# Kernel optimization log

Measured on AMD Instinct MI355X. Metric: run time of the kernel, lower is better.

## Reference

```python
import jax, jax.numpy as jnp
import numpy as np
from jax import lax

KERNEL_SIZE = 3  # matches init_kwargs


def setup_inputs() -> dict:
    key = jax.random.key(0)
    heatmap = jax.random.normal(key, (8, 16, 512, 512), dtype=jnp.float32)
    return {"heatmap": heatmap, "max_peaks": 262144}


def reference(heatmap, max_peaks):
    """Peak detection: local maxima of 3x3 neighborhood that are > 0.

    Returns:
      peaks:  (B, max_peaks, 3) float32, rows [x, y, confidence] packed in
              (channel, row-major) order (identical ordering to the torch
              per-channel torch.where + cat), zero-padded after counts[b].
      counts: (B,) int32, number of valid peak rows per batch item.
    """
    k = KERNEL_SIZE
    pad = (k - 1) // 2
    # max_pool2d(stride=1, padding=pad) pads with -inf implicitly
    max_pooled = lax.reduce_window(
        heatmap, -jnp.inf, lax.max,
        window_dimensions=(1, 1, k, k),
        window_strides=(1, 1, 1, 1),
        padding=[(0, 0), (0, 0), (pad, pad), (pad, pad)],
    )
    peak_mask = (heatmap == max_pooled) & (heatmap > 0)

    B, C, H, W = heatmap.shape
    n = C * H * W
    flat_mask = peak_mask.reshape(B, n)
    flat_val = heatmap.reshape(B, n)

    # Stream compaction: stable argsort moves valid flat indices (in order)
    # to the front; invalid entries get sentinel key n.
    idx = jnp.arange(n, dtype=jnp.int32)
    keys = jnp.where(flat_mask, idx, jnp.int32(n))
    order = jnp.argsort(keys, axis=1)[:, :max_peaks]  # (B, max_peaks)

    valid = jnp.take_along_axis(flat_mask, order, axis=1)
    conf = jnp.take_along_axis(flat_val, order, axis=1)
    x = (order % W).astype(heatmap.dtype)
    y = ((order // W) % H).astype(heatmap.dtype)

    peaks = jnp.where(valid[..., None], jnp.stack([x, y, conf], axis=-1), 0.0)
    counts = flat_mask.sum(axis=1).astype(jnp.int32)
    return peaks, counts
```

## Files before the change

kernel.cpp:

```cpp
#include <hip/hip_runtime.h>


namespace {
constexpr int kB = 8;
constexpr int kC = 16;
constexpr int kH = 512;
constexpr int kW = 512;
constexpr int kNPB = kC * kH * kW;
constexpr int kMaxPeaks = 262144;
constexpr int kRows = 8;
constexpr int kStripsPerBatch = kC * (kH / kRows);
constexpr int kNStrips = kB * kStripsPerBatch;
constexpr int kWPB = 4;
constexpr int kTPB = 64 * kWPB;
constexpr long long kPeaksElems = (long long)kB * kMaxPeaks * 3;
constexpr float kNeg = -3.402823466e38f;
}

__device__ __forceinline__ float fmax3(float a, float b, float c) {
  return fmaxf(fmaxf(a, b), c);
}

__global__ void __launch_bounds__(kTPB)
peak_count_kernel(const float* __restrict__ hm,
                  unsigned long long* __restrict__ bmw,
                  int* __restrict__ cnts) {
  const int t = threadIdx.x, lane = t & 63, wv = t >> 6;
  const int s = blockIdx.x * kWPB + wv;
  const int b = s >> 10;
  const int si = s & 1023;
  const int c = si >> 6;
  const int y0 = (si & 63) * kRows;
  const float* rp = hm + (long long)b * kNPB + c * (kH * kW) + y0 * kW + lane * 8;

  float a[10][8];
#pragma unroll
  for (int i = 1; i <= 8; ++i) {
    const float4 q0 = *reinterpret_cast<const float4*>(rp + (i - 1) * kW);
    const float4 q1 = *reinterpret_cast<const float4*>(rp + (i - 1) * kW + 4);
    a[i][0] = q0.x; a[i][1] = q0.y; a[i][2] = q0.z; a[i][3] = q0.w;
    a[i][4] = q1.x; a[i][5] = q1.y; a[i][6] = q1.z; a[i][7] = q1.w;
  }
  if (y0 > 0) {
    const float4 q0 = *reinterpret_cast<const float4*>(rp - kW);
    const float4 q1 = *reinterpret_cast<const float4*>(rp - kW + 4);
    a[0][0] = q0.x; a[0][1] = q0.y; a[0][2] = q0.z; a[0][3] = q0.w;
    a[0][4] = q1.x; a[0][5] = q1.y; a[0][6] = q1.z; a[0][7] = q1.w;
  } else {
#pragma unroll
    for (int j = 0; j < 8; ++j) a[0][j] = kNeg;
  }
  if (y0 + kRows < kH) {
    const float4 q0 = *reinterpret_cast<const float4*>(rp + 8 * kW);
    const float4 q1 = *reinterpret_cast<const float4*>(rp + 8 * kW + 4);
    a[9][0] = q0.x; a[9][1] = q0.y; a[9][2] = q0.z; a[9][3] = q0.w;
    a[9][4] = q1.x; a[9][5] = q1.y; a[9][6] = q1.z; a[9][7] = q1.w;
  } else {
#pragma unroll
    for (int j = 0; j < 8; ++j) a[9][j] = kNeg;
  }

  unsigned long long myword = 0;
  int scnt = 0;
#pragma unroll
  for (int r = 0; r < kRows; ++r) {
    float cm[8];
#pragma unroll
    for (int j = 0; j < 8; ++j) cm[j] = fmax3(a[r][j], a[r + 1][j], a[r + 2][j]);
    float hl = __shfl_up(cm[7], 1, 64);
    float hr = __shfl_down(cm[0], 1, 64);
    if (lane == 0) hl = kNeg;
    if (lane == 63) hr = kNeg;
    float m[8];
    m[0] = fmax3(hl, cm[0], cm[1]);
#pragma unroll
    for (int j = 1; j < 7; ++j) m[j] = fmax3(cm[j - 1], cm[j], cm[j + 1]);
    m[7] = fmax3(cm[6], cm[7], hr);
#pragma unroll
    for (int j = 0; j < 8; ++j) {
      const float v = a[r + 1][j];
      const unsigned long long wj = __ballot((v == m[j]) && (v > 0.0f));
      scnt += (int)__popcll(wj);
      if (lane == r * 8 + j) myword = wj;
    }
  }
  bmw[(long long)s * 64 + lane] = myword;
  if (lane == 0) cnts[s] = scnt;
}

__global__ void __launch_bounds__(kTPB)
peak_write_kernel(const float* __restrict__ hm,
                  const unsigned long long* __restrict__ bmw,
                  const int* __restrict__ cnts,
                  float* __restrict__ out) {
  __shared__ int s_pre[kWPB], s_tot[kWPB], s_c[kWPB];
  __shared__ unsigned long long s_w[kWPB][64];
  const int t = threadIdx.x, lane = t & 63, wv = t >> 6;
  const int g = blockIdx.x;
  const int b = g >> 8;
  const int g0 = (g & 255) * kWPB;
  const int* cb = cnts + b * kStripsPerBatch;

  const int4 c4 = *reinterpret_cast<const int4*>(cb + t * 4);
  const int idx0 = t * 4;
  int tot = c4.x + c4.y + c4.z + c4.w;
  int pre = (idx0 < g0) ? tot : 0;
  if (idx0 == g0) { s_c[0] = c4.x; s_c[1] = c4.y; s_c[2] = c4.z; s_c[3] = c4.w; }
#pragma unroll
  for (int d = 32; d >= 1; d >>= 1) {
    pre += __shfl_down(pre, d, 64);
    tot += __shfl_down(tot, d, 64);
  }
  if (lane == 0) { s_pre[wv] = pre; s_tot[wv] = tot; }
  __syncthreads();
  const int base = s_pre[0] + s_pre[1] + s_pre[2] + s_pre[3];
  if (g0 == 0 && t == 0)
    out[kPeaksElems + b] =
        (float)(s_tot[0] + s_tot[1] + s_tot[2] + s_tot[3]);

  int off0 = base;
  for (int k = 0; k < wv; ++k) off0 += s_c[k];
  if (off0 >= kMaxPeaks) return;

  const int s = b * kStripsPerBatch + g0 + wv;
  const int si = g0 + wv, c = si >> 6, y0 = (si & 63) * kRows;
  const float* rp = hm + (long long)b * kNPB + c * (kH * kW) + y0 * kW + lane * 8;

  float4 cv[kRows][2];
#pragma unroll
  for (int r = 0; r < kRows; ++r) {
    cv[r][0] = *reinterpret_cast<const float4*>(rp + r * kW);
    cv[r][1] = *reinterpret_cast<const float4*>(rp + r * kW + 4);
  }

  s_w[wv][lane] = bmw[(long long)s * 64 + lane];

  const unsigned long long pm = (lane == 0) ? 0ull : (~0ull >> (64 - lane));
  int rbase = off0;
  float* pb = out + (long long)b * kMaxPeaks * 3;
#pragma unroll
  for (int r = 0; r < kRows; ++r) {
    unsigned long long w[8];
#pragma unroll
    for (int j = 0; j < 8; ++j) w[j] = s_w[wv][r * 8 + j];
    int lexcl = 0, rowcnt = 0;
#pragma unroll
    for (int j = 0; j < 8; ++j) {
      lexcl += (int)__popcll(w[j] & pm);
      rowcnt += (int)__popcll(w[j]);
    }
    int rank = rbase + lexcl;
    const float vv[8] = {cv[r][0].x, cv[r][0].y, cv[r][0].z, cv[r][0].w,
                         cv[r][1].x, cv[r][1].y, cv[r][1].z, cv[r][1].w};
    const float fy = (float)(y0 + r);
#pragma unroll
    for (int j = 0; j < 8; ++j) {
      const int f = (int)((w[j] >> lane) & 1);
      if (f && rank < kMaxPeaks) {
        float* o = pb + (long long)rank * 3;
        o[0] = (float)(lane * 8 + j);
        o[1] = fy;
        o[2] = vv[j];
      }
      rank += f;
    }
    rbase += rowcnt;
    if (rbase >= kMaxPeaks) break;
  }
}

extern "C" void kernel_launch(void* const* d_in, const int* in_sizes, int n_in,
                              void* d_out, int out_size, void* d_ws, size_t ws_size,
                              hipStream_t stream) {
  const float* hm = (const float*)d_in[0];
  float* out = (float*)d_out;

  unsigned long long* bmw = (unsigned long long*)d_ws;
  int* cnts = (int*)(bmw + (long long)kNStrips * 64);

  peak_count_kernel<<<kNStrips / kWPB, kTPB, 0, stream>>>(hm, bmw, cnts);
  peak_write_kernel<<<kNStrips / kWPB, kTPB, 0, stream>>>(hm, bmw, cnts, out);
}
```

Baseline: 220.3 us.

## Fuse count and write kernels with a grid-wide atomic barrier

Merges the peak-count and peak-write kernels into one persistent-style kernel. Each block handles 16 strips and keeps the peak bitmasks in shared memory instead of global memory. It publishes per-strip counts globally, then waits at a spin barrier on an atomic counter before doing the prefix sum and scatter. This removes the second launch and the bitmask round trip through global memory. The risks are deadlock if all 512 blocks are not co-resident, spin overhead at the barrier, and an extra memset launch.

Measured after the change: 310.2 us. +40.8%, slower.

```diff
diff --git a/kernel.cpp b/kernel.cpp
--- a/kernel.cpp
+++ b/kernel.cpp
@@ -11,8 +11,11 @@
 constexpr int kRows = 8;
 constexpr int kStripsPerBatch = kC * (kH / kRows);
 constexpr int kNStrips = kB * kStripsPerBatch;
-constexpr int kWPB = 4;
-constexpr int kTPB = 64 * kWPB;
+constexpr int kSPB = 16;
+constexpr int kNBlocks = kNStrips / kSPB;
+constexpr int kBlocksPerBatch = kStripsPerBatch / kSPB;
+constexpr int kTPB = 256;
+constexpr int kCntStride = 32;
 constexpr long long kPeaksElems = (long long)kB * kMaxPeaks * 3;
 constexpr float kNeg = -3.402823466e38f;
 }
@@ -21,151 +24,171 @@
   return fmaxf(fmaxf(a, b), c);
 }
 
-__global__ void __launch_bounds__(kTPB)
-peak_count_kernel(const float* __restrict__ hm,
-                  unsigned long long* __restrict__ bmw,
-                  int* __restrict__ cnts) {
+__global__ void __launch_bounds__(kTPB, 2)
+peak_fused(const float* __restrict__ hm, unsigned* __restrict__ bar,
+           int* __restrict__ cntg, float* __restrict__ out) {
+  __shared__ unsigned long long s_w[kSPB][64];
+  __shared__ int s_cnt[kSPB];
+  __shared__ int s_red[kTPB / 64], s_red2[kTPB / 64];
+
   const int t = threadIdx.x, lane = t & 63, wv = t >> 6;
-  const int s = blockIdx.x * kWPB + wv;
-  const int b = s >> 10;
-  const int si = s & 1023;
-  const int c = si >> 6;
-  const int y0 = (si & 63) * kRows;
-  const float* rp = hm + (long long)b * kNPB + c * (kH * kW) + y0 * kW + lane * 8;
-
-  float a[10][8];
-#pragma unroll
-  for (int i = 1; i <= 8; ++i) {
-    const float4 q0 = *reinterpret_cast<const float4*>(rp + (i - 1) * kW);
-    const float4 q1 = *reinterpret_cast<const float4*>(rp + (i - 1) * kW + 4);
-    a[i][0] = q0.x; a[i][1] = q0.y; a[i][2] = q0.z; a[i][3] = q0.w;
-    a[i][4] = q1.x; a[i][5] = q1.y; a[i][6] = q1.z; a[i][7] = q1.w;
-  }
-  if (y0 > 0) {
-    const float4 q0 = *reinterpret_cast<const float4*>(rp - kW);
-    const float4 q1 = *reinterpret_cast<const float4*>(rp - kW + 4);
-    a[0][0] = q0.x; a[0][1] = q0.y; a[0][2] = q0.z; a[0][3] = q0.w;
-    a[0][4] = q1.x; a[0][5] = q1.y; a[0][6] = q1.z; a[0][7] = q1.w;
-  } else {
-#pragma unroll
-    for (int j = 0; j < 8; ++j) a[0][j] = kNeg;
-  }
-  if (y0 + kRows < kH) {
-    const float4 q0 = *reinterpret_cast<const float4*>(rp + 8 * kW);
-    const float4 q1 = *reinterpret_cast<const float4*>(rp + 8 * kW + 4);
-    a[9][0] = q0.x; a[9][1] = q0.y; a[9][2] = q0.z; a[9][3] = q0.w;
-    a[9][4] = q1.x; a[9][5] = q1.y; a[9][6] = q1.z; a[9][7] = q1.w;
-  } else {
-#pragma unroll
-    for (int j = 0; j < 8; ++j) a[9][j] = kNeg;
-  }
-
-  unsigned long long myword = 0;
-  int scnt = 0;
-#pragma unroll
-  for (int r = 0; r < kRows; ++r) {
-    float cm[8];
-#pragma unroll
-    for (int j = 0; j < 8; ++j) cm[j] = fmax3(a[r][j], a[r + 1][j], a[r + 2][j]);
-    float hl = __shfl_up(cm[7], 1, 64);
-    float hr = __shfl_down(cm[0], 1, 64);
-    if (lane == 0) hl = kNeg;
-    if (lane == 63) hr = kNeg;
-    float m[8];
-    m[0] = fmax3(hl, cm[0], cm[1]);
-#pragma unroll
-    for (int j = 1; j < 7; ++j) m[j] = fmax3(cm[j - 1], cm[j], cm[j + 1]);
-    m[7] = fmax3(cm[6], cm[7], hr);
-#pragma unroll
-    for (int j = 0; j < 8; ++j) {
-      const float v = a[r + 1][j];
-      const unsigned long long wj = __ballot((v == m[j]) && (v > 0.0f));
-      scnt += (int)__popcll(wj);
-      if (lane == r * 8 + j) myword = wj;
-    }
-  }
-  bmw[(long long)s * 64 + lane] = myword;
-  if (lane == 0) cnts[s] = scnt;
-}
-
-__global__ void __launch_bounds__(kTPB)
-peak_write_kernel(const float* __restrict__ hm,
-                  const unsigned long long* __restrict__ bmw,
-                  const int* __restrict__ cnts,
-                  float* __restrict__ out) {
-  __shared__ int s_pre[kWPB], s_tot[kWPB], s_c[kWPB];
-  __shared__ unsigned long long s_w[kWPB][64];
-  const int t = threadIdx.x, lane = t & 63, wv = t >> 6;
-  const int g = blockIdx.x;
-  const int b = g >> 8;
-  const int g0 = (g & 255) * kWPB;
-  const int* cb = cnts + b * kStripsPerBatch;
-
-  const int4 c4 = *reinterpret_cast<const int4*>(cb + t * 4);
-  const int idx0 = t * 4;
-  int tot = c4.x + c4.y + c4.z + c4.w;
-  int pre = (idx0 < g0) ? tot : 0;
-  if (idx0 == g0) { s_c[0] = c4.x; s_c[1] = c4.y; s_c[2] = c4.z; s_c[3] = c4.w; }
-#pragma unroll
-  for (int d = 32; d >= 1; d >>= 1) {
-    pre += __shfl_down(pre, d, 64);
-    tot += __shfl_down(tot, d, 64);
-  }
-  if (lane == 0) { s_pre[wv] = pre; s_tot[wv] = tot; }
-  __syncthreads();
-  const int base = s_pre[0] + s_pre[1] + s_pre[2] + s_pre[3];
-  if (g0 == 0 && t == 0)
+  const int blk = blockIdx.x;
+  const int b = blk / kBlocksPerBatch;
+  const int jb = blk & (kBlocksPerBatch - 1);
+
+  for (int k = 0; k < kSPB / 4; ++k) {
+    const int m = wv * 4 + k;
+    const int si = (blk * kSPB + m) & (kStripsPerBatch - 1);
+    const int c = si >> 6;
+    const int y0 = (si & 63) * kRows;
+    const float* rp =
+        hm + (long long)b * kNPB + c * (kH * kW) + y0 * kW + lane * 8;
+
+    float a[10][8];
+#pragma unroll
+    for (int i = 1; i <= 8; ++i) {
+      const float4 q0 = *reinterpret_cast<const float4*>(rp + (i - 1) * kW);
+      const float4 q1 = *reinterpret_cast<const float4*>(rp + (i - 1) * kW + 4);
+      a[i][0] = q0.x; a[i][1] = q0.y; a[i][2] = q0.z; a[i][3] = q0.w;
+      a[i][4] = q1.x; a[i][5] = q1.y; a[i][6] = q1.z; a[i][7] = q1.w;
+    }
+    if (y0 > 0) {
+      const float4 q0 = *reinterpret_cast<const float4*>(rp - kW);
+      const float4 q1 = *reinterpret_cast<const float4*>(rp - kW + 4);
+      a[0][0] = q0.x; a[0][1] = q0.y; a[0][2] = q0.z; a[0][3] = q0.w;
+      a[0][4] = q1.x; a[0][5] = q1.y; a[0][6] = q1.z; a[0][7] = q1.w;
+    } else {
+#pragma unroll
+      for (int jj = 0; jj < 8; ++jj) a[0][jj] = kNeg;
+    }
+    if (y0 + kRows < kH) {
+      const float4 q0 = *reinterpret_cast<const float4*>(rp + 8 * kW);
+      const float4 q1 = *reinterpret_cast<const float4*>(rp + 8 * kW + 4);
+      a[9][0] = q0.x; a[9][1] = q0.y; a[9][2] = q0.z; a[9][3] = q0.w;
+      a[9][4] = q1.x; a[9][5] = q1.y; a[9][6] = q1.z; a[9][7] = q1.w;
+    } else {
+#pragma unroll
+      for (int jj = 0; jj < 8; ++jj) a[9][jj] = kNeg;
+    }
+
+    unsigned long long myword = 0;
+    int scnt = 0;
+#pragma unroll
+    for (int r = 0; r < kRows; ++r) {
+      float cm[8];
+#pragma unroll
+      for (int jj = 0; jj < 8; ++jj)
+        cm[jj] = fmax3(a[r][jj], a[r + 1][jj], a[r + 2][jj]);
+      float hl = __shfl_up(cm[7], 1, 64);
+      float hr = __shfl_down(cm[0], 1, 64);
+      if (lane == 0) hl = kNeg;
+      if (lane == 63) hr = kNeg;
+      float mx[8];
+      mx[0] = fmax3(hl, cm[0], cm[1]);
+#pragma unroll
+      for (int jj = 1; jj < 7; ++jj) mx[jj] = fmax3(cm[jj - 1], cm[jj], cm[jj + 1]);
+      mx[7] = fmax3(cm[6], cm[7], hr);
+#pragma unroll
+      for (int jj = 0; jj < 8; ++jj) {
+        const float v = a[r + 1][jj];
+        const unsigned long long wj = __ballot((v == mx[jj]) && (v > 0.0f));
+        scnt += (int)__popcll(wj);
+        if (lane == r * 8 + jj) myword = wj;
+      }
+    }
+    s_w[m][lane] = myword;
+    if (lane == 0) s_cnt[m] = scnt;
+  }
+  __syncthreads();
+  if (t < kSPB) cntg[blk * kCntStride + t] = s_cnt[t];
+
+  __syncthreads();
+  if (t == 0) {
+    __threadfence();
+    const unsigned arrived =
+        __hip_atomic_fetch_add(bar, 1u, __ATOMIC_ACQ_REL,
+                               __HIP_MEMORY_SCOPE_AGENT) + 1;
+    if (arrived < (unsigned)kNBlocks) {
+      while (__hip_atomic_load(bar, __ATOMIC_ACQUIRE,
+                               __HIP_MEMORY_SCOPE_AGENT) < (unsigned)kNBlocks)
+        __builtin_amdgcn_s_sleep(8);
+    }
+    __threadfence();
+  }
+  __syncthreads();
+
+  {
+    const int j = t >> 2, i4 = (t & 3) * 4;
+    const int4 c4 = *reinterpret_cast<const int4*>(
+        cntg + (b * kBlocksPerBatch + j) * kCntStride + i4);
+    int tot = c4.x + c4.y + c4.z + c4.w;
+    int pre = (j < jb) ? tot : 0;
+#pragma unroll
+    for (int d = 32; d >= 1; d >>= 1) {
+      pre += __shfl_down(pre, d, 64);
+      tot += __shfl_down(tot, d, 64);
+    }
+    if (lane == 0) { s_red[wv] = pre; s_red2[wv] = tot; }
+  }
+  __syncthreads();
+  const int base = s_red[0] + s_red[1] + s_red[2] + s_red[3];
+  if (jb == 0 && t == 0)
     out[kPeaksElems + b] =
-        (float)(s_tot[0] + s_tot[1] + s_tot[2] + s_tot[3]);
+        (float)(s_red2[0] + s_red2[1] + s_red2[2] + s_red2[3]);
 
   int off0 = base;
-  for (int k = 0; k < wv; ++k) off0 += s_c[k];
-  if (off0 >= kMaxPeaks) return;
-
-  const int s = b * kStripsPerBatch + g0 + wv;
-  const int si = g0 + wv, c = si >> 6, y0 = (si & 63) * kRows;
-  const float* rp = hm + (long long)b * kNPB + c * (kH * kW) + y0 * kW + lane * 8;
-
-  float4 cv[kRows][2];
-#pragma unroll
-  for (int r = 0; r < kRows; ++r) {
-    cv[r][0] = *reinterpret_cast<const float4*>(rp + r * kW);
-    cv[r][1] = *reinterpret_cast<const float4*>(rp + r * kW + 4);
-  }
-
-  s_w[wv][lane] = bmw[(long long)s * 64 + lane];
+  for (int i = 0; i < wv * 4; ++i) off0 += s_cnt[i];
 
   const unsigned long long pm = (lane == 0) ? 0ull : (~0ull >> (64 - lane));
-  int rbase = off0;
   float* pb = out + (long long)b * kMaxPeaks * 3;
-#pragma unroll
-  for (int r = 0; r < kRows; ++r) {
-    unsigned long long w[8];
-#pragma unroll
-    for (int j = 0; j < 8; ++j) w[j] = s_w[wv][r * 8 + j];
-    int lexcl = 0, rowcnt = 0;
-#pragma unroll
-    for (int j = 0; j < 8; ++j) {
-      lexcl += (int)__popcll(w[j] & pm);
-      rowcnt += (int)__popcll(w[j]);
-    }
-    int rank = rbase + lexcl;
-    const float vv[8] = {cv[r][0].x, cv[r][0].y, cv[r][0].z, cv[r][0].w,
-                         cv[r][1].x, cv[r][1].y, cv[r][1].z, cv[r][1].w};
-    const float fy = (float)(y0 + r);
-#pragma unroll
-    for (int j = 0; j < 8; ++j) {
-      const int f = (int)((w[j] >> lane) & 1);
-      if (f && rank < kMaxPeaks) {
-        float* o = pb + (long long)rank * 3;
-        o[0] = (float)(lane * 8 + j);
-        o[1] = fy;
-        o[2] = vv[j];
+  for (int k = 0; k < kSPB / 4; ++k) {
+    const int m = wv * 4 + k;
+    if (off0 < kMaxPeaks) {
+      const int si = (blk * kSPB + m) & (kStripsPerBatch - 1);
+      const int c = si >> 6;
+      const int y0 = (si & 63) * kRows;
+      const float* rp =
+          hm + (long long)b * kNPB + c * (kH * kW) + y0 * kW + lane * 8;
+
+      float4 cv[kRows][2];
+#pragma unroll
+      for (int r = 0; r < kRows; ++r) {
+        cv[r][0] = *reinterpret_cast<const float4*>(rp + r * kW);
+        cv[r][1] = *reinterpret_cast<const float4*>(rp + r * kW + 4);
       }
-      rank += f;
-    }
-    rbase += rowcnt;
-    if (rbase >= kMaxPeaks) break;
+
+      int rbase = off0;
+#pragma unroll
+      for (int r = 0; r < kRows; ++r) {
+        unsigned long long w[8];
+#pragma unroll
+        for (int jj = 0; jj < 8; ++jj) w[jj] = s_w[m][r * 8 + jj];
+        int lexcl = 0, rowcnt = 0;
+#pragma unroll
+        for (int jj = 0; jj < 8; ++jj) {
+          lexcl += (int)__popcll(w[jj] & pm);
+          rowcnt += (int)__popcll(w[jj]);
+        }
+        int rank = rbase + lexcl;
+        const float vv[8] = {cv[r][0].x, cv[r][0].y, cv[r][0].z, cv[r][0].w,
+                             cv[r][1].x, cv[r][1].y, cv[r][1].z, cv[r][1].w};
+        const float fy = (float)(y0 + r);
+#pragma unroll
+        for (int jj = 0; jj < 8; ++jj) {
+          const int f = (int)((w[jj] >> lane) & 1);
+          if (f && rank < kMaxPeaks) {
+            float* o = pb + (long long)rank * 3;
+            o[0] = (float)(lane * 8 + jj);
+            o[1] = fy;
+            o[2] = vv[jj];
+          }
+          rank += f;
+        }
+        rbase += rowcnt;
+        if (rbase >= kMaxPeaks) break;
+      }
+    }
+    off0 += s_cnt[m];
   }
 }
 
@@ -175,9 +198,9 @@
   const float* hm = (const float*)d_in[0];
   float* out = (float*)d_out;
 
-  unsigned long long* bmw = (unsigned long long*)d_ws;
-  int* cnts = (int*)(bmw + (long long)kNStrips * 64);
-
-  peak_count_kernel<<<kNStrips / kWPB, kTPB, 0, stream>>>(hm, bmw, cnts);
-  peak_write_kernel<<<kNStrips / kWPB, kTPB, 0, stream>>>(hm, bmw, cnts, out);
-}
+  unsigned* bar = (unsigned*)d_ws;
+  int* cntg = (int*)((char*)d_ws + 128);
+
+  hipMemsetAsync(d_ws, 0, 128, stream);
+  peak_fused<<<kNBlocks, kTPB, 0, stream>>>(hm, bar, cntg, out);
+}
```
